# Optimization experiments

Hardware: AMD Instinct MI355X
Metric: run time of the kernel (lower is better)

The kernel has to match this reference:

```python
import jax, jax.numpy as jnp
import numpy as np

B, N, H, KRATE = 128, 400, 128, 0.2
EPS = 1e-9


def setup_inputs() -> dict:
    key = jax.random.key(0)
    ks = jax.random.split(key, 16)
    # correlation-like input: symmetric, values in (-1,1), unit diagonal
    x = jax.random.normal(ks[0], (B, N, N), dtype=jnp.float32)
    x = jnp.tanh(0.3 * x)
    x = 0.5 * (x + x.transpose(0, 2, 1))
    eye = jnp.eye(N, dtype=jnp.float32)
    x = x * (1.0 - eye) + eye

    def lin(k, fan_in, shape):
        return jax.random.normal(k, shape, dtype=jnp.float32) / np.sqrt(fan_in).astype(np.float32)

    return {
        "x": x,
        "slength": jnp.full((B,), 100, dtype=jnp.int32),
        # AE denoiser (num_of_node=N, hidden=H)
        "enc1_w": lin(ks[1], N, (N, H)), "enc1_b": jnp.zeros((H,), jnp.float32),
        "enc2_w": lin(ks[2], N, (N, H)), "enc2_b": jnp.zeros((H,), jnp.float32),
        "dec2_w": lin(ks[3], H, (H, N)), "dec2_b": jnp.zeros((N,), jnp.float32),
        "dec1_w": lin(ks[4], H, (H, N)), "dec1_b": jnp.zeros((N,), jnp.float32),
        # GCN predictor
        "gcn1_w": lin(ks[5], N, (N, H)), "gcn1_b": jnp.zeros((H,), jnp.float32),
        "gcn2_w": lin(ks[6], H, (H, H)), "gcn2_b": jnp.zeros((H,), jnp.float32),
        # classification head Linear(128 -> 2)
        "fc_w": lin(ks[7], H, (H, 2)), "fc_b": jnp.zeros((2,), jnp.float32),
    }


def reference(x, slength, enc1_w, enc1_b, enc2_w, enc2_b, dec2_w, dec2_b,
              dec1_w, dec1_b, gcn1_w, gcn1_b, gcn2_w, gcn2_b, fc_w, fc_b):
    eye = jnp.eye(N, dtype=x.dtype)

    # fisher transform + normalize by [0,0] entry
    xf = 0.5 * jnp.log((1.0 + x + EPS) / (1.0 - x + EPS))
    xf = xf / xf[:, 0, 0][:, None, None]

    # --- DA / AE denoiser: deltax = AE(xf), symmetrized ---
    out1 = jax.nn.relu(jnp.einsum('bij,jh->bih', xf, enc1_w) + enc1_b).transpose(0, 2, 1)  # [B,H,N]
    out2 = jax.nn.relu(jnp.einsum('bhn,nk->bhk', out1, enc2_w) + enc2_b)                   # [B,H,H]
    out2 = jax.nn.relu(jnp.einsum('bhk,kn->bhn', out2, dec2_w) + dec2_b + out1)            # [B,H,N]
    out2 = out2.transpose(0, 2, 1)                                                         # [B,N,H]
    delta = jnp.einsum('bnh,hm->bnm', out2, dec1_w) + dec1_b                               # [B,N,N]
    delta = 0.5 * (delta + delta.transpose(0, 2, 1))
    x2 = xf + delta * (1.0 - eye)

    # --- predictor on detached x2 ---
    xp = jax.lax.stop_gradient(x2)

    # topk sparsification at rate 0.2 over flattened NxN per sample
    k = int(N * N * KRATE)
    flat = xp.reshape(B, N * N)
    _, idx = jax.lax.top_k(flat, k)
    mask = jnp.zeros((B, N * N), xp.dtype).at[jnp.arange(B)[:, None], idx].set(1.0)
    A = xp * mask.reshape(B, N, N)

    # GCN norm (PyG gcn_norm with add_remaining_self_loops, fill=1)
    diag = jnp.diagonal(A, axis1=1, axis2=2)
    A = A + eye[None] * jnp.where(diag == 0.0, 1.0, 0.0)[:, :, None]
    deg = A.sum(axis=1)                      # scatter of edge weight on col index
    dinv = deg ** -0.5
    dinv = jnp.where(jnp.isinf(dinv), 0.0, dinv)
    An = dinv[:, :, None] * A * dinv[:, None, :]  # An[b,i,j] = dinv[i]*A[i,j]*dinv[j]

    # GCNConv1 -> ReLU -> GCNConv2 (aggregate onto col/target index)
    h = jax.nn.relu(jnp.einsum('bij,bif->bjf', An, xp @ gcn1_w) + gcn1_b)  # [B,N,H]
    h = jnp.einsum('bij,bif->bjf', An, h @ gcn2_w) + gcn2_b                # [B,N,H]

    pooled = h.mean(axis=1)                  # mean over nodes -> [B,H]
    out = jax.nn.relu(pooled) @ fc_w + fc_b  # [B,2]
    return out
```

## Files before the change

kernel.cpp:

```cpp
#include <hip/hip_runtime.h>
#include <hip/hip_bf16.h>
#include <math.h>

#define BATCH 128
#define NNODE 400
#define HID   128
#define NN    (NNODE*NNODE)
#define KSEL  32000
#define EQCAP 1024
#define EPSF  1e-9f
#define TSPLIT 8
#define SEG   (NN / TSPLIT)
#define NT    7
#define KC400 14
#define FRAGS (KC400*4096)
#define PLA   57344

__device__ __forceinline__ unsigned tokey(float f) {
  unsigned u = __float_as_uint(f);
  return (u & 0x80000000u) ? ~u : (u | 0x80000000u);
}

__device__ __forceinline__ short f2bf(float f) {
  unsigned u = __float_as_uint(f);
  u += 0x7fffu + ((u >> 16) & 1u);
  return (short)(u >> 16);
}
__device__ __forceinline__ float bf2f(short s) {
  return __uint_as_float(((unsigned)(unsigned short)s) << 16);
}

__device__ __forceinline__ float xfhw(float xv, float cmul) {
  float la = __builtin_amdgcn_logf(1.0f + xv + EPSF);
  float lb = __builtin_amdgcn_logf(1.0f - xv + EPSF);
  return (la - lb) * cmul;
}

typedef __attribute__((ext_vector_type(8))) short s8v;
typedef __attribute__((ext_vector_type(4))) short s4v;
typedef __attribute__((ext_vector_type(4))) float f4v;

#define BK 16
#define LP 68

template<bool AT, bool BIAS, bool RES, bool RELU, bool TS>
__global__ void __launch_bounds__(256) gemm64(
    const float* __restrict__ A, long sA, int lda,
    const float* __restrict__ B, long sB, int ldb,
    const float* __restrict__ bias,
    const float* __restrict__ Res, long sRes,
    float* __restrict__ C, long sC, int ldc,
    int M, int Nc, int K)
{
  __shared__ float As[BK][LP];
  __shared__ float Bs[BK][LP];
  const int bz = blockIdx.z;
  A += (size_t)bz * sA;
  B += (size_t)bz * sB;
  C += (size_t)bz * sC;
  const float* Rp = RES ? (Res + (size_t)bz * sRes) : nullptr;

  const int n0 = blockIdx.x * 64;
  const int m0 = blockIdx.y * 64;
  const int tid = threadIdx.x;
  const int tx = tid & 15, ty = tid >> 4;
  const bool edgeM = (m0 + 64 > M);
  const bool edgeN = (n0 + 64 > Nc);

  float acc[4][4];
#pragma unroll
  for (int i = 0; i < 4; ++i)
#pragma unroll
    for (int j = 0; j < 4; ++j) acc[i][j] = 0.f;

  for (int k0 = 0; k0 < K; k0 += BK) {
    if (!AT) {
      const int m = tid & 63, g = tid >> 6;
      if (!edgeM) {
        const float4 v = *(const float4*)(A + (size_t)(m0 + m) * lda + k0 + 4 * g);
        As[4 * g + 0][m] = v.x; As[4 * g + 1][m] = v.y;
        As[4 * g + 2][m] = v.z; As[4 * g + 3][m] = v.w;
      } else {
        const int gm = m0 + m;
        const bool ok = gm < M;
#pragma unroll
        for (int j = 0; j < 4; ++j)
          As[4 * g + j][m] = ok ? A[(size_t)gm * lda + k0 + 4 * g + j] : 0.f;
      }
    } else {
      const int k = tid >> 4, mg = tid & 15;
      if (!edgeM) {
        const float4 v = *(const float4*)(A + (size_t)(k0 + k) * lda + m0 + 4 * mg);
        *(float4*)&As[k][4 * mg] = v;
      } else {
#pragma unroll
        for (int j = 0; j < 4; ++j) {
          const int gm = m0 + 4 * mg + j;
          As[k][4 * mg + j] = (gm < M) ? A[(size_t)(k0 + k) * lda + gm] : 0.f;
        }
      }
    }
    {
      const int k = tid >> 4, ng = tid & 15;
      if (!edgeN) {
        const float4 v = *(const float4*)(B + (size_t)(k0 + k) * ldb + n0 + 4 * ng);
        *(float4*)&Bs[k][4 * ng] = v;
      } else {
#pragma unroll
        for (int j = 0; j < 4; ++j) {
          const int gn = n0 + 4 * ng + j;
          Bs[k][4 * ng + j] = (gn < Nc) ? B[(size_t)(k0 + k) * ldb + gn] : 0.f;
        }
      }
    }
    __syncthreads();
#pragma unroll
    for (int kk = 0; kk < BK; ++kk) {
      const float4 a = *(const float4*)&As[kk][ty << 2];
      const float4 b = *(const float4*)&Bs[kk][tx << 2];
      const float av[4] = {a.x, a.y, a.z, a.w};
      const float bv[4] = {b.x, b.y, b.z, b.w};
#pragma unroll
      for (int i = 0; i < 4; ++i)
#pragma unroll
        for (int j = 0; j < 4; ++j) acc[i][j] += av[i] * bv[j];
    }
    __syncthreads();
  }

#pragma unroll
  for (int i = 0; i < 4; ++i) {
    const int m = m0 + (ty << 2) + i;
    if (m >= M) continue;
#pragma unroll
    for (int j = 0; j < 4; ++j) {
      const int n = n0 + (tx << 2) + j;
      if (n >= Nc) continue;
      float v = acc[i][j];
      if (BIAS) v += bias[n];
      const size_t loc = TS ? ((size_t)n * ldc + m) : ((size_t)m * ldc + n);
      if (RES) v += Rp[loc];
      if (RELU) v = fmaxf(v, 0.f);
      C[loc] = v;
    }
  }
}

__global__ void bsplit5(
    const float* __restrict__ gcn1_w, const float* __restrict__ gcn2_w,
    const float* __restrict__ enc1_w, const float* __restrict__ enc2_w,
    const float* __restrict__ dec1_w,
    short* __restrict__ w1frag, short* __restrict__ w2frag,
    short* __restrict__ e1frag, short* __restrict__ e2frag,
    short* __restrict__ dfrag) {
  const float* W; short* out; int K, Kpad, N, Npad;
  switch (blockIdx.y) {
    case 0: W = gcn1_w; out = w1frag; K = NNODE; Kpad = 448; N = HID;   Npad = 128; break;
    case 1: W = gcn2_w; out = w2frag; K = HID;   Kpad = 128; N = HID;   Npad = 128; break;
    case 2: W = enc1_w; out = e1frag; K = NNODE; Kpad = 448; N = HID;   Npad = 128; break;
    case 3: W = enc2_w; out = e2frag; K = NNODE; Kpad = 448; N = HID;   Npad = 128; break;
    default: W = dec1_w; out = dfrag; K = HID;   Kpad = 128; N = NNODE; Npad = 448; break;
  }
  int t = blockIdx.x * 256 + threadIdx.x;
  if (t >= Kpad * Npad) return;
  int k = t / Npad, n = t - k * Npad;
  float v = (k < K && n < N) ? W[(size_t)k * N + n] : 0.f;
  short hi = f2bf(v);
  short lo = f2bf(v - bf2f(hi));
  int ntiles = Npad >> 4;
  size_t idx = (((size_t)(k >> 5) * ntiles + (n >> 4)) * 64
                + (((k >> 3) & 3) * 16 + (n & 15))) * 8 + (k & 7);
  size_t PL = (size_t)(Kpad >> 5) * ntiles * 512;
  out[idx] = hi;
  out[PL + idx] = lo;
}

template<bool AT, bool FRAG, bool BIAS, bool RELU, bool SCL, bool TS, bool XF>
__global__ void __launch_bounds__(256) mfgemm(
    const float* __restrict__ A, long sA, int lda,
    const short* __restrict__ Bf, long sB, int kc,
    const float* __restrict__ bias,
    const float* __restrict__ scl,
    float* __restrict__ Cf, long sCf, int ldc,
    short* __restrict__ Cfrag, long sCfrag, int okc,
    const float* __restrict__ denomp, float* __restrict__ xfout,
    int M, int K)
{
  __shared__ float As[64][68];
  const int bz = blockIdx.y;
  A += (size_t)bz * sA;
  Bf += (size_t)bz * sB;
  if (SCL) scl += (size_t)bz * NNODE;
  if (!FRAG) Cf += (size_t)bz * sCf;
  else       Cfrag += (size_t)bz * sCfrag;
  if (XF) xfout += (size_t)bz * sA;
  const float cmul = XF ? (0.34657359027997264f / denomp[bz]) : 0.f;

  const int tid = threadIdx.x;
  const int lane = tid & 63, wave = tid >> 6;
  const int wqm = wave >> 1, wqn = wave & 1;
  const int quad = lane >> 4, l15 = lane & 15;
  const int m0 = blockIdx.x * 64;

  f4v acc[2][4];
#pragma unroll
  for (int i = 0; i < 2; ++i)
#pragma unroll
    for (int j = 0; j < 4; ++j) acc[i][j] = (f4v){0.f, 0.f, 0.f, 0.f};

  const int nstage = (K + 63) >> 6;
  for (int st = 0; st < nstage; ++st) {
    const int k0 = st << 6;
    if (st) __syncthreads();
    if (!AT) {
      const int mrow = tid >> 4;
      const int k4 = (tid & 15) << 2;
#pragma unroll
      for (int u = 0; u < 4; ++u) {
        const int m = mrow + (u << 4);
        const int gm = m0 + m, gk = k0 + k4;
        float4 v = {0.f, 0.f, 0.f, 0.f};
        if (gm < M) {
          if (gk + 4 <= K) {
            float4 xv = *(const float4*)(A + (size_t)gm * lda + gk);
            if (XF) {
              v.x = xfhw(xv.x, cmul);
              v.y = xfhw(xv.y, cmul);
              v.z = xfhw(xv.z, cmul);
              v.w = xfhw(xv.w, cmul);
              *(float4*)(xfout + (size_t)gm * lda + gk) = v;
            } else v = xv;
          } else {
            float* pv = (float*)&v;
#pragma unroll
            for (int j = 0; j < 4; ++j)
              if (gk + j < K) {
                float xv = A[(size_t)gm * lda + gk + j];
                if (XF) {
                  pv[j] = xfhw(xv, cmul);
                  xfout[(size_t)gm * lda + gk + j] = pv[j];
                } else pv[j] = xv;
              }
          }
        }
        *(float4*)&As[m][k4] = v;
      }
    } else {
      const int kk = tid >> 4;
      const int m4 = (tid & 15) << 2;
#pragma unroll
      for (int u = 0; u < 4; ++u) {
        const int gk = k0 + kk + (u << 4);
        float4 v = {0.f, 0.f, 0.f, 0.f};
        if (gk < K) {
          if (m0 + m4 + 4 <= M) v = *(const float4*)(A + (size_t)gk * lda + m0 + m4);
          else {
            float* pv = (float*)&v;
#pragma unroll
            for (int j = 0; j < 4; ++j)
              if (m0 + m4 + j < M) pv[j] = A[(size_t)gk * lda + m0 + m4 + j];
          }
        }
        As[m4 + 0][kk + (u << 4)] = v.x;
        As[m4 + 1][kk + (u << 4)] = v.y;
        As[m4 + 2][kk + (u << 4)] = v.z;
        As[m4 + 3][kk + (u << 4)] = v.w;
      }
    }
    __syncthreads();

#pragma unroll
    for (int c2 = 0; c2 < 2; ++c2) {
      const int c = (st << 1) + c2;
      s8v bhi[4], blo[4];
#pragma unroll
      for (int nt = 0; nt < 4; ++nt) {
        const int ntg = (wqn << 2) + nt;
        const size_t off = (((size_t)c * 8 + ntg) * 64 + lane) * 8;
        bhi[nt] = *(const s8v*)(Bf + off);
        blo[nt] = *(const s8v*)(Bf + (size_t)kc * 4096 + off);
      }
#pragma unroll
      for (int mt = 0; mt < 2; ++mt) {
        const int row = (wqm << 5) + (mt << 4) + l15;
        const int kof = (c2 << 5) + (quad << 3);
        const f4v a0 = *(const f4v*)&As[row][kof];
        const f4v a1 = *(const f4v*)&As[row][kof + 4];
        s8v ah, al;
#pragma unroll
        for (int j = 0; j < 4; ++j) {
          short h0 = f2bf(a0[j]); ah[j] = h0; al[j] = f2bf(a0[j] - bf2f(h0));
          short h1 = f2bf(a1[j]); ah[j + 4] = h1; al[j + 4] = f2bf(a1[j] - bf2f(h1));
        }
#pragma unroll
        for (int nt = 0; nt < 4; ++nt) {
          acc[mt][nt] = __builtin_amdgcn_mfma_f32_16x16x32_bf16(ah, bhi[nt], acc[mt][nt], 0, 0, 0);
          acc[mt][nt] = __builtin_amdgcn_mfma_f32_16x16x32_bf16(ah, blo[nt], acc[mt][nt], 0, 0, 0);
          acc[mt][nt] = __builtin_amdgcn_mfma_f32_16x16x32_bf16(al, bhi[nt], acc[mt][nt], 0, 0, 0);
        }
      }
    }
  }

  if (TS) {
    for (int nh = 0; nh < 2; ++nh) {
      __syncthreads();
      if (wqn == nh) {
#pragma unroll
        for (int mt = 0; mt < 2; ++mt)
#pragma unroll
          for (int nt = 0; nt < 4; ++nt) {
            const int tn = (nt << 4) + l15;
            const int n  = (wqn << 6) + tn;
            const int mc = (wqm << 5) + (mt << 4) + (quad << 2);
            const f4v a = acc[mt][nt];
#pragma unroll
            for (int reg = 0; reg < 4; ++reg) {
              float v = a[reg];
              if (SCL) v *= scl[m0 + mc + reg];
              if (BIAS) v += bias[n];
              if (RELU) v = fmaxf(v, 0.f);
              As[tn][mc + reg] = v;
            }
          }
      }
      __syncthreads();
      const int row = tid >> 2, cq = tid & 3;
#pragma unroll
      for (int u = 0; u < 4; ++u) {
        const int col = (cq + (u << 2)) << 2;
        if (m0 + col + 4 <= M) {
          const float4 v = *(const float4*)&As[row][col];
          *(float4*)(Cf + (size_t)((nh << 6) + row) * ldc + m0 + col) = v;
        }
      }
    }
    return;
  }

#pragma unroll
  for (int mt = 0; mt < 2; ++mt) {
    const int mb = m0 + (wqm << 5) + (mt << 4) + (quad << 2);
#pragma unroll
    for (int nt = 0; nt < 4; ++nt) {
      const int n = (wqn << 6) + (nt << 4) + l15;
      const f4v a = acc[mt][nt];
      if (!FRAG) {
#pragma unroll
        for (int reg = 0; reg < 4; ++reg) {
          const int m = mb + reg;
          if (m < M) {
            float v = a[reg];
            if (SCL) v *= scl[m];
            if (BIAS) v += bias[n];
            if (RELU) v = fmaxf(v, 0.f);
            Cf[(size_t)m * ldc + n] = v;
          }
        }
      } else {
        s4v h4, l4;
#pragma unroll
        for (int reg = 0; reg < 4; ++reg) {
          const int m = mb + reg;
          float v = (m < M) ? (SCL ? a[reg] * scl[m] : a[reg]) : 0.f;
          short hh = f2bf(v);
          h4[reg] = hh; l4[reg] = f2bf(v - bf2f(hh));
        }
        const int chunkT = mb >> 5, quadT = (mb >> 3) & 3, jT0 = mb & 7;
        const size_t off = (((size_t)chunkT * 8 + (wqn << 2) + nt) * 64
                            + quadT * 16 + l15) * 8 + jT0;
        *(s4v*)(Cfrag + off) = h4;
        *(s4v*)(Cfrag + (size_t)okc * 4096 + off) = l4;
      }
    }
  }
}

__global__ void __launch_bounds__(256) g4mf(
    const float* __restrict__ o1,
    const short* __restrict__ wfrag,
    const float* __restrict__ bias,
    float* __restrict__ xf,
    unsigned* __restrict__ ghist)
{
  __shared__ float D2[64][68];
  __shared__ unsigned hist[2048];
  const int b = blockIdx.y;
  int p = blockIdx.x, bi = 0;
  while (p >= NT - bi) { p -= NT - bi; ++bi; }
  const int bj = bi + p;
  const int I0 = bi * 64, J0 = bj * 64;
  const bool diag = (bi == bj);

  o1 += (size_t)b * HID * NNODE;
  xf += (size_t)b * NN;
  unsigned* gh = ghist + (size_t)b * 4096;

  const int tid = threadIdx.x;
  const int lane = tid & 63, wave = tid >> 6;
  const int wq = wave & 1;
  const bool d1 = wave < 2;
  const int Bt = (d1 ? bj : bi) * 4;
  const int quad = lane >> 4, l15 = lane & 15;
  const int M0 = d1 ? I0 : J0;

  for (int i = tid; i < 2048; i += 256) hist[i] = 0u;

  f4v acc[2][4];
#pragma unroll
  for (int i = 0; i < 2; ++i)
#pragma unroll
    for (int j = 0; j < 4; ++j) acc[i][j] = (f4v){0.f, 0.f, 0.f, 0.f};

  const int gm0 = M0 + (wq << 5) + l15;

  for (int c = 0; c < 4; ++c) {
    const int k0 = c << 5;
    s8v bhi[4], blo[4];
#pragma unroll
    for (int nt = 0; nt < 4; ++nt) {
      const int ntg = Bt + nt;
      const size_t off = (((size_t)c * 28 + ntg) * 64 + lane) * 8;
      bhi[nt] = *(const s8v*)(wfrag + off);
      blo[nt] = *(const s8v*)(wfrag + PLA + off);
    }
#pragma unroll
    for (int mt = 0; mt < 2; ++mt) {
      const int gm = gm0 + (mt << 4);
      float av[8];
      if (gm < NNODE) {
        const float* cp = o1 + (size_t)(k0 + (quad << 3)) * NNODE + gm;
#pragma unroll
        for (int j = 0; j < 8; ++j) av[j] = cp[(size_t)j * NNODE];
      } else {
#pragma unroll
        for (int j = 0; j < 8; ++j) av[j] = 0.f;
      }
      s8v ah, al;
#pragma unroll
      for (int j = 0; j < 8; ++j) {
        short h = f2bf(av[j]); ah[j] = h; al[j] = f2bf(av[j] - bf2f(h));
      }
#pragma unroll
      for (int nt = 0; nt < 4; ++nt) {
        acc[mt][nt] = __builtin_amdgcn_mfma_f32_16x16x32_bf16(ah, bhi[nt], acc[mt][nt], 0, 0, 0);
        acc[mt][nt] = __builtin_amdgcn_mfma_f32_16x16x32_bf16(ah, blo[nt], acc[mt][nt], 0, 0, 0);
        acc[mt][nt] = __builtin_amdgcn_mfma_f32_16x16x32_bf16(al, bhi[nt], acc[mt][nt], 0, 0, 0);
      }
    }
  }

  if (!d1) {
#pragma unroll
    for (int mt = 0; mt < 2; ++mt) {
      const int mb = (wq << 5) + (mt << 4) + (quad << 2);
#pragma unroll
      for (int nt = 0; nt < 4; ++nt) {
        const int nn = (nt << 4) + l15;
        const f4v a = acc[mt][nt];
#pragma unroll
        for (int reg = 0; reg < 4; ++reg) D2[mb + reg][nn] = a[reg];
      }
    }
  }
  __syncthreads();

  if (d1) {
    const unsigned w = diag ? 1u : 2u;
#pragma unroll
    for (int mt = 0; mt < 2; ++mt) {
      const int a0 = (wq << 5) + (mt << 4) + (quad << 2);
#pragma unroll
      for (int nt = 0; nt < 4; ++nt) {
        const int nn = (nt << 4) + l15;
        const int gj = J0 + nn;
        const f4v d1v = acc[mt][nt];
        const f4v d2t = *(const f4v*)&D2[nn][a0];
        f4v vv;
#pragma unroll
        for (int reg = 0; reg < 4; ++reg) {
          const int gi = I0 + a0 + reg;
          float v = 0.f;
          if (gi < NNODE && gj < NNODE) {
            v = xf[(size_t)gi * NNODE + gj];
            if (gi != gj)
              v += 0.5f * (d1v[reg] + d2t[reg] + bias[gj] + bias[gi]);
            const unsigned bin = tokey(v) >> 20;
            atomicAdd(&hist[bin >> 1], w << ((bin & 1) << 4));
          }
          vv[reg] = v;
        }
#pragma unroll
        for (int reg = 0; reg < 4; ++reg) {
          const int gi = I0 + a0 + reg;
          if (gi < NNODE && gj < NNODE) xf[(size_t)gi * NNODE + gj] = vv[reg];
        }
        if (!diag && gj < NNODE && (I0 + a0 + 4 <= NNODE)) {
          *(float4*)(xf + (size_t)gj * NNODE + I0 + a0) = *(float4*)&vv;
        }
      }
    }
  }
  __syncthreads();
  for (int i = tid; i < 2048; i += 256) {
    const unsigned v = hist[i];
    const unsigned lo = v & 0xFFFFu, hi = v >> 16;
    if (lo) atomicAdd(&gh[2 * i], lo);
    if (hi) atomicAdd(&gh[2 * i + 1], hi);
  }
}

__global__ void tzd(const float* __restrict__ x, unsigned* __restrict__ ghist,
                    unsigned* __restrict__ sprefix, int* __restrict__ sk,
                    int* __restrict__ eqcnt, float* __restrict__ deg,
                    float* __restrict__ denom, unsigned* __restrict__ ccnt2) {
  int t = blockIdx.x * 256 + threadIdx.x;
  if (t < BATCH * 4096) ghist[t] = 0u;
  if (t < BATCH) {
    sprefix[t] = 0u; sk[t] = KSEL; eqcnt[t] = 0;
    float v = x[(size_t)t * NN];
    denom[t] = 0.5f * logf((1.0f + v + EPSF) / (1.0f - v + EPSF));
  }
  if (t < BATCH * TSPLIT) ccnt2[t] = 0u;
  if (t < BATCH * NNODE) deg[t] = 0.f;
}

__global__ void __launch_bounds__(256) thistA(const float* __restrict__ x2,
                                              const unsigned* __restrict__ sprefix,
                                              unsigned* __restrict__ ghist,
                                              unsigned* __restrict__ cand,
                                              unsigned* __restrict__ ccnt2) {
  __shared__ unsigned h[4096];
  __shared__ unsigned lcnt;
  const int b  = blockIdx.y;
  const int sb = blockIdx.x;
  const int tid = threadIdx.x;
  for (int i = tid; i < 4096; i += 256) h[i] = 0u;
  if (tid == 0) lcnt = 0u;
  __syncthreads();

  const unsigned prefix = sprefix[b];
  unsigned* cb = cand + (size_t)b * NN + (size_t)sb * SEG;
  const float4* p4 = (const float4*)(x2 + (size_t)b * NN);
  const int i0 = sb * (SEG / 4), i1 = i0 + (SEG / 4);
  for (int i = i0 + tid; i < i1; i += 256) {
    float4 v = p4[i];
    unsigned kk[4] = {tokey(v.x), tokey(v.y), tokey(v.z), tokey(v.w)};
#pragma unroll
    for (int q = 0; q < 4; ++q) {
      const unsigned key = kk[q];
      if ((key & 0xFFF00000u) == prefix) {
        atomicAdd(&h[(key >> 8) & 4095u], 1u);
        const unsigned pos = atomicAdd(&lcnt, 1u);
        cb[pos] = key;
      }
    }
  }
  __syncthreads();
  for (int i = tid; i < 4096; i += 256) {
    unsigned s = h[i];
    if (s) atomicAdd(&ghist[(size_t)b * 4096 + i], s);
  }
  if (tid == 0) ccnt2[b * TSPLIT + sb] = lcnt;
}

template<int SH>
__global__ void __launch_bounds__(256) tpick12(unsigned* __restrict__ ghist,
                                               unsigned* __restrict__ sprefix,
                                               int* __restrict__ sk) {
  const int b = blockIdx.x;
  __shared__ unsigned h[4096];
  __shared__ unsigned csum[256];
  unsigned* gh = ghist + (size_t)b * 4096;
  unsigned local = 0;
#pragma unroll
  for (int u = 0; u < 16; ++u) {
    unsigned v = gh[threadIdx.x * 16 + u];
    h[threadIdx.x * 16 + u] = v;
    local += v;
  }
  csum[threadIdx.x] = local;
  __syncthreads();
  if (threadIdx.x == 0) {
    int k = sk[b];
    int bin = 0;
    for (int ch = 255; ch >= 0; --ch) {
      int S = (int)csum[ch];
      if (S >= k) {
        for (int bb = ch * 16 + 15; bb >= ch * 16; --bb) {
          int c = (int)h[bb];
          if (c >= k) { bin = bb; break; }
          k -= c;
        }
        break;
      }
      k -= S;
    }
    sprefix[b] = sprefix[b] | ((unsigned)bin << SH);
    sk[b] = k;
  }
#pragma unroll
  for (int u = 0; u < 16; ++u) gh[threadIdx.x * 16 + u] = 0u;
}

__global__ void __launch_bounds__(256) thistC(const unsigned* __restrict__ cand,
                                              const unsigned* __restrict__ ccnt2,
                                              const unsigned* __restrict__ sprefix,
                                              const int* __restrict__ sk,
                                              unsigned* __restrict__ tau,
                                              int* __restrict__ rrem) {
  __shared__ unsigned h[8][256];
  const int b = blockIdx.x;
  const int tid = threadIdx.x;
  for (int i = tid; i < 8 * 256; i += 256) ((unsigned*)h)[i] = 0u;
  __syncthreads();
  const unsigned prefix = sprefix[b];
  const int rep = tid & 7;
  for (int sb = 0; sb < TSPLIT; ++sb) {
    const unsigned n = ccnt2[b * TSPLIT + sb];
    const unsigned* cp = cand + (size_t)b * NN + (size_t)sb * SEG;
    for (unsigned i = tid; i < n; i += 256) {
      const unsigned key = cp[i];
      if ((key & 0xFFFFFF00u) == prefix) atomicAdd(&h[rep][key & 255u], 1u);
    }
  }
  __syncthreads();
  if (tid < 256) {
    const unsigned s = h[0][tid] + h[1][tid] + h[2][tid] + h[3][tid]
                     + h[4][tid] + h[5][tid] + h[6][tid] + h[7][tid];
    h[0][tid] = s;
  }
  __syncthreads();
  if (tid == 0) {
    int k = sk[b];
    unsigned byte = 0u;
    for (int bin = 255; bin >= 0; --bin) {
      int c = (int)h[0][bin];
      if (c >= k) { byte = (unsigned)bin; break; }
      k -= c;
    }
    tau[b] = prefix | byte;
    rrem[b] = k;
  }
}

__global__ void __launch_bounds__(256) build_kc(
    const float* __restrict__ x2, const unsigned* __restrict__ tau,
    float* __restrict__ A, float* __restrict__ deg,
    int* __restrict__ eqcnt, int* __restrict__ eqidx) {
  __shared__ float cs[NNODE];
  const int b = blockIdx.y, rg = blockIdx.x;
  const int tid = threadIdx.x;
  for (int i = tid; i < NNODE; i += 256) cs[i] = 0.f;
  __syncthreads();
  const unsigned tk = tau[b];
  const size_t base = (size_t)b * NN + (size_t)rg * 6400;
  for (int u = 0; u < 25; ++u) {
    const int t = u * 256 + tid;
    const float v = x2[base + t];
    const unsigned key = tokey(v);
    const float a = (key > tk) ? v : 0.f;
    A[base + t] = a;
    if (key == tk) {
      int p = atomicAdd(&eqcnt[b], 1);
      if (p < EQCAP) eqidx[b * EQCAP + p] = rg * 6400 + t;
    }
    if (a != 0.f) atomicAdd(&cs[t % NNODE], a);
  }
  __syncthreads();
  for (int j = tid; j < NNODE; j += 256)
    if (cs[j] != 0.f) atomicAdd(&deg[b * NNODE + j], cs[j]);
}

__global__ void __launch_bounds__(256) eqdinv(
    float* __restrict__ A, const float* __restrict__ x2,
    float* __restrict__ deg, float* __restrict__ dinv,
    const int* __restrict__ eqcnt, const int* __restrict__ eqidx,
    const int* __restrict__ rrem) {
  const int b = blockIdx.x;
  int cnt = eqcnt[b]; if (cnt > EQCAP) cnt = EQCAP;
  const int r = rrem[b];
  for (int t = threadIdx.x; t < cnt; t += 256) {
    int idx = eqidx[b * EQCAP + t];
    int rank = 0;
    for (int u = 0; u < cnt; ++u) rank += (eqidx[b * EQCAP + u] < idx) ? 1 : 0;
    if (rank < r) {
      float v = x2[(size_t)b * NN + idx];
      A[(size_t)b * NN + idx] = v;
      atomicAdd(&deg[b * NNODE + idx % NNODE], v);
    }
  }
  __syncthreads();
  for (int j = threadIdx.x; j < NNODE; j += 256) {
    float d = deg[b * NNODE + j];
    size_t o = (size_t)b * NN + (size_t)j * NNODE + j;
    if (A[o] == 0.f) { A[o] = 1.0f; d += 1.0f; }
    dinv[b * NNODE + j] = (d == 0.f) ? 0.f : 1.0f / sqrtf(d);
  }
}

__global__ void head_k(const float* __restrict__ h2, const float* __restrict__ fc_w,
                       const float* __restrict__ fc_b, float* __restrict__ out) {
  int b = blockIdx.x;
  int f = threadIdx.x;
  float s = 0.f;
  const float* p = h2 + (size_t)b * NNODE * HID + f;
  for (int j = 0; j < NNODE; ++j) s += p[(size_t)j * HID];
  float pv = fmaxf(s / (float)NNODE, 0.f);
  __shared__ float r0[128], r1[128];
  r0[f] = pv * fc_w[f * 2 + 0];
  r1[f] = pv * fc_w[f * 2 + 1];
  __syncthreads();
  for (int sft = 64; sft > 0; sft >>= 1) {
    if (f < sft) { r0[f] += r0[f + sft]; r1[f] += r1[f + sft]; }
    __syncthreads();
  }
  if (f == 0) {
    out[b * 2 + 0] = r0[0] + fc_b[0];
    out[b * 2 + 1] = r1[0] + fc_b[1];
  }
}

extern "C" void kernel_launch(void* const* d_in, const int* in_sizes, int n_in,
                              void* d_out, int out_size, void* d_ws, size_t ws_size,
                              hipStream_t stream) {
  const float* x      = (const float*)d_in[0];
  const float* enc1_w = (const float*)d_in[2];
  const float* enc1_b = (const float*)d_in[3];
  const float* enc2_w = (const float*)d_in[4];
  const float* enc2_b = (const float*)d_in[5];
  const float* dec2_w = (const float*)d_in[6];
  const float* dec2_b = (const float*)d_in[7];
  const float* dec1_w = (const float*)d_in[8];
  const float* dec1_b = (const float*)d_in[9];
  const float* gcn1_w = (const float*)d_in[10];
  const float* gcn1_b = (const float*)d_in[11];
  const float* gcn2_w = (const float*)d_in[12];
  const float* gcn2_b = (const float*)d_in[13];
  const float* fc_w   = (const float*)d_in[14];
  const float* fc_b   = (const float*)d_in[15];
  float* out = (float*)d_out;
  (void)in_sizes; (void)n_in; (void)out_size; (void)ws_size;

  float* ws = (float*)d_ws;
  size_t off = 0;
  auto take = [&](size_t n) { float* p = ws + off; off += (n + 63) & ~(size_t)63; return p; };
  float* xf   = take((size_t)BATCH * NN);
  float* dl   = take((size_t)BATCH * NN);
  float* o1   = take((size_t)BATCH * HID * NNODE);
  float* o2   = take((size_t)BATCH * HID * HID);
  float* hbuf = take((size_t)BATCH * NNODE * HID);
  float* denom = take(BATCH);
  float* dinv  = take((size_t)BATCH * NNODE);
  float* deg   = take((size_t)BATCH * NNODE);
  unsigned* tau = (unsigned*)take(BATCH);
  int* rrem  = (int*)take(BATCH);
  int* eqcnt = (int*)take(BATCH);
  int* eqidx = (int*)take((size_t)BATCH * EQCAP);
  unsigned* ghist   = (unsigned*)take((size_t)BATCH * 4096);
  unsigned* sprefix = (unsigned*)take(BATCH);
  int*      sk      = (int*)take(BATCH);
  unsigned* ccnt2   = (unsigned*)take((size_t)BATCH * TSPLIT);
  short* w1frag = (short*)take((size_t)FRAGS + 64);
  short* w2frag = (short*)take((size_t)4 * 4096 + 64);
  short* e1frag = (short*)take((size_t)FRAGS + 64);
  short* e2frag = (short*)take((size_t)FRAGS + 64);
  short* dfrag  = (short*)take((size_t)PLA + 64);
  short* xwfrag = (short*)o1;
  unsigned* cand = (unsigned*)dl;
  const long sXW = 2L * FRAGS;

  tzd<<<2048, 256, 0, stream>>>(x, ghist, sprefix, sk, eqcnt, deg, denom, ccnt2);
  bsplit5<<<dim3(224, 5), 256, 0, stream>>>(gcn1_w, gcn2_w, enc1_w, enc2_w, dec1_w,
                                            w1frag, w2frag, e1frag, e2frag, dfrag);

  mfgemm<false, false, true, true, false, true, true><<<dim3(7, BATCH), 256, 0, stream>>>(
      x, NN, NNODE, e1frag, 0, KC400, enc1_b, nullptr,
      o1, (long)HID * NNODE, NNODE, nullptr, 0, 0, denom, xf, NNODE, NNODE);
  mfgemm<false, false, true, true, false, false, false><<<dim3(2, BATCH), 256, 0, stream>>>(
      o1, (long)HID * NNODE, NNODE, e2frag, 0, KC400, enc2_b, nullptr,
      o2, (long)HID * HID, HID, nullptr, 0, 0, nullptr, nullptr, HID, NNODE);
  gemm64<false, true, true, true, false><<<dim3(7, 2, BATCH), 256, 0, stream>>>(
      o2, (long)HID * HID, HID, dec2_w, 0, NNODE, dec2_b,
      o1, (long)HID * NNODE, o1, (long)HID * NNODE, NNODE, HID, NNODE, HID);

  g4mf<<<dim3(NT * (NT + 1) / 2, BATCH), 256, 0, stream>>>(o1, dfrag, dec1_b, xf, ghist);

  tpick12<20><<<BATCH, 256, 0, stream>>>(ghist, sprefix, sk);
  thistA<<<dim3(TSPLIT, BATCH), 256, 0, stream>>>(xf, sprefix, ghist, cand, ccnt2);
  tpick12<8><<<BATCH, 256, 0, stream>>>(ghist, sprefix, sk);
  thistC<<<BATCH, 256, 0, stream>>>(cand, ccnt2, sprefix, sk, tau, rrem);

  build_kc<<<dim3(25, BATCH), 256, 0, stream>>>(xf, tau, dl, deg, eqcnt, eqidx);
  eqdinv<<<BATCH, 256, 0, stream>>>(dl, xf, deg, dinv, eqcnt, eqidx, rrem);

  mfgemm<false, true, false, false, true, false, false><<<dim3(7, BATCH), 256, 0, stream>>>(
      xf, NN, NNODE, w1frag, 0, KC400, nullptr, dinv,
      nullptr, 0, 128, xwfrag, sXW, KC400, nullptr, nullptr, NNODE, NNODE);
  mfgemm<true, false, true, true, true, false, false><<<dim3(7, BATCH), 256, 0, stream>>>(
      dl, NN, NNODE, xwfrag, sXW, KC400, gcn1_b, dinv,
      hbuf, (long)NNODE * HID, HID, nullptr, 0, 0, nullptr, nullptr, NNODE, NNODE);
  mfgemm<false, true, false, false, true, false, false><<<dim3(7, BATCH), 256, 0, stream>>>(
      hbuf, (long)NNODE * HID, HID, w2frag, 0, 4, nullptr, dinv,
      nullptr, 0, 128, xwfrag, sXW, KC400, nullptr, nullptr, NNODE, HID);
  mfgemm<true, false, true, false, true, false, false><<<dim3(7, BATCH), 256, 0, stream>>>(
      dl, NN, NNODE, xwfrag, sXW, KC400, gcn2_b, dinv,
      hbuf, (long)NNODE * HID, HID, nullptr, 0, 0, nullptr, nullptr, NNODE, NNODE);

  head_k<<<BATCH, HID, 0, stream>>>(hbuf, fc_w, fc_b, out);
}
```

Before: 694.2 us.

## Fuse top-k mask build and degree accumulation into the X·W1 GEMM load

Removes the separate build_kc pass by doing the threshold masking, tie collection and per-column degree accumulation inside the A-tile load of the xf·W1 GEMM, since that GEMM already streams all of xf. The dinv row scaling that this GEMM used to apply is moved to the A-operand load of the aggregation GEMMs (DSCL), because dinv is not yet available when the fused kernel runs. This saves one full read of the x2 matrix and a launch. In exchange the GEMM does atomics during tile loads and the later GEMMs do extra multiplies.

```diff
diff --git a/kernel.cpp b/kernel.cpp
--- a/kernel.cpp
+++ b/kernel.cpp
@@ -175,7 +175,8 @@
   out[PL + idx] = lo;
 }
 
-template<bool AT, bool FRAG, bool BIAS, bool RELU, bool SCL, bool TS, bool XF>
+template<bool AT, bool FRAG, bool BIAS, bool RELU, bool SCL, bool TS, bool XF,
+         bool MASK, bool DSCL>
 __global__ void __launch_bounds__(256) mfgemm(
     const float* __restrict__ A, long sA, int lda,
     const short* __restrict__ Bf, long sB, int kc,
@@ -184,9 +185,13 @@
     float* __restrict__ Cf, long sCf, int ldc,
     short* __restrict__ Cfrag, long sCfrag, int okc,
     const float* __restrict__ denomp, float* __restrict__ xfout,
+    const unsigned* __restrict__ taup, float* __restrict__ Aout,
+    float* __restrict__ degp, int* __restrict__ eqcntp,
+    int* __restrict__ eqidxp, const float* __restrict__ dsclp,
     int M, int K)
 {
   __shared__ float As[64][68];
+  __shared__ float cs[MASK ? NNODE : 1];
   const int bz = blockIdx.y;
   A += (size_t)bz * sA;
   Bf += (size_t)bz * sB;
@@ -195,12 +200,21 @@
   else       Cfrag += (size_t)bz * sCfrag;
   if (XF) xfout += (size_t)bz * sA;
   const float cmul = XF ? (0.34657359027997264f / denomp[bz]) : 0.f;
+  const unsigned tk = MASK ? taup[bz] : 0u;
+  if (MASK) { Aout += (size_t)bz * NN; degp += (size_t)bz * NNODE;
+              eqcntp += bz; eqidxp += (size_t)bz * EQCAP; }
+  if (DSCL) dsclp += (size_t)bz * NNODE;
 
   const int tid = threadIdx.x;
   const int lane = tid & 63, wave = tid >> 6;
   const int wqm = wave >> 1, wqn = wave & 1;
   const int quad = lane >> 4, l15 = lane & 15;
   const int m0 = blockIdx.x * 64;
+
+  if (MASK) {
+    for (int i = tid; i < NNODE; i += 256) cs[i] = 0.f;
+    __syncthreads();
+  }
 
   f4v acc[2][4];
 #pragma unroll
@@ -230,6 +244,23 @@
               v.w = xfhw(xv.w, cmul);
               *(float4*)(xfout + (size_t)gm * lda + gk) = v;
             } else v = xv;
+            if (MASK) {
+              float4 av;
+              float* pa = (float*)&av;
+              const float* px = (const float*)&v;
+#pragma unroll
+              for (int j = 0; j < 4; ++j) {
+                const unsigned key = tokey(px[j]);
+                float a = (key > tk) ? px[j] : 0.f;
+                if (key == tk) {
+                  int p = atomicAdd(eqcntp, 1);
+                  if (p < EQCAP) eqidxp[p] = gm * NNODE + gk + j;
+                }
+                if (a != 0.f) atomicAdd(&cs[gk + j], a);
+                pa[j] = a;
+              }
+              *(float4*)(Aout + (size_t)gm * NNODE + gk) = av;
+            }
           } else {
             float* pv = (float*)&v;
 #pragma unroll
@@ -240,6 +271,16 @@
                   pv[j] = xfhw(xv, cmul);
                   xfout[(size_t)gm * lda + gk + j] = pv[j];
                 } else pv[j] = xv;
+                if (MASK) {
+                  const unsigned key = tokey(pv[j]);
+                  float a = (key > tk) ? pv[j] : 0.f;
+                  if (key == tk) {
+                    int p = atomicAdd(eqcntp, 1);
+                    if (p < EQCAP) eqidxp[p] = gm * NNODE + gk + j;
+                  }
+                  if (a != 0.f) atomicAdd(&cs[gk + j], a);
+                  Aout[(size_t)gm * NNODE + gk + j] = a;
+                }
               }
           }
         }
@@ -253,12 +294,18 @@
         const int gk = k0 + kk + (u << 4);
         float4 v = {0.f, 0.f, 0.f, 0.f};
         if (gk < K) {
-          if (m0 + m4 + 4 <= M) v = *(const float4*)(A + (size_t)gk * lda + m0 + m4);
-          else {
+          const float ds = DSCL ? dsclp[gk] : 1.f;
+          if (m0 + m4 + 4 <= M) {
+            v = *(const float4*)(A + (size_t)gk * lda + m0 + m4);
+            if (DSCL) { v.x *= ds; v.y *= ds; v.z *= ds; v.w *= ds; }
+          } else {
             float* pv = (float*)&v;
 #pragma unroll
             for (int j = 0; j < 4; ++j)
-              if (m0 + m4 + j < M) pv[j] = A[(size_t)gk * lda + m0 + m4 + j];
+              if (m0 + m4 + j < M) {
+                float t = A[(size_t)gk * lda + m0 + m4 + j];
+                pv[j] = DSCL ? t * ds : t;
+              }
           }
         }
         As[m4 + 0][kk + (u << 4)] = v.x;
@@ -299,6 +346,14 @@
           acc[mt][nt] = __builtin_amdgcn_mfma_f32_16x16x32_bf16(al, bhi[nt], acc[mt][nt], 0, 0, 0);
         }
       }
+    }
+  }
+
+  if (MASK) {
+    __syncthreads();
+    for (int j = tid; j < NNODE; j += 256) {
+      const float s = cs[j];
+      if (s != 0.f) atomicAdd(&degp[j], s);
     }
   }
 
@@ -642,34 +697,6 @@
     tau[b] = prefix | byte;
     rrem[b] = k;
   }
-}
-
-__global__ void __launch_bounds__(256) build_kc(
-    const float* __restrict__ x2, const unsigned* __restrict__ tau,
-    float* __restrict__ A, float* __restrict__ deg,
-    int* __restrict__ eqcnt, int* __restrict__ eqidx) {
-  __shared__ float cs[NNODE];
-  const int b = blockIdx.y, rg = blockIdx.x;
-  const int tid = threadIdx.x;
-  for (int i = tid; i < NNODE; i += 256) cs[i] = 0.f;
-  __syncthreads();
-  const unsigned tk = tau[b];
-  const size_t base = (size_t)b * NN + (size_t)rg * 6400;
-  for (int u = 0; u < 25; ++u) {
-    const int t = u * 256 + tid;
-    const float v = x2[base + t];
-    const unsigned key = tokey(v);
-    const float a = (key > tk) ? v : 0.f;
-    A[base + t] = a;
-    if (key == tk) {
-      int p = atomicAdd(&eqcnt[b], 1);
-      if (p < EQCAP) eqidx[b * EQCAP + p] = rg * 6400 + t;
-    }
-    if (a != 0.f) atomicAdd(&cs[t % NNODE], a);
-  }
-  __syncthreads();
-  for (int j = tid; j < NNODE; j += 256)
-    if (cs[j] != 0.f) atomicAdd(&deg[b * NNODE + j], cs[j]);
 }
 
 __global__ void __launch_bounds__(256) eqdinv(
@@ -774,12 +801,14 @@
   bsplit5<<<dim3(224, 5), 256, 0, stream>>>(gcn1_w, gcn2_w, enc1_w, enc2_w, dec1_w,
                                             w1frag, w2frag, e1frag, e2frag, dfrag);
 
-  mfgemm<false, false, true, true, false, true, true><<<dim3(7, BATCH), 256, 0, stream>>>(
+  mfgemm<false, false, true, true, false, true, true, false, false><<<dim3(7, BATCH), 256, 0, stream>>>(
       x, NN, NNODE, e1frag, 0, KC400, enc1_b, nullptr,
-      o1, (long)HID * NNODE, NNODE, nullptr, 0, 0, denom, xf, NNODE, NNODE);
-  mfgemm<false, false, true, true, false, false, false><<<dim3(2, BATCH), 256, 0, stream>>>(
+      o1, (long)HID * NNODE, NNODE, nullptr, 0, 0, denom, xf,
+      nullptr, nullptr, nullptr, nullptr, nullptr, nullptr, NNODE, NNODE);
+  mfgemm<false, false, true, true, false, false, false, false, false><<<dim3(2, BATCH), 256, 0, stream>>>(
       o1, (long)HID * NNODE, NNODE, e2frag, 0, KC400, enc2_b, nullptr,
-      o2, (long)HID * HID, HID, nullptr, 0, 0, nullptr, nullptr, HID, NNODE);
+      o2, (long)HID * HID, HID, nullptr, 0, 0, nullptr, nullptr,
+      nullptr, nullptr, nullptr, nullptr, nullptr, nullptr, HID, NNODE);
   gemm64<false, true, true, true, false><<<dim3(7, 2, BATCH), 256, 0, stream>>>(
       o2, (long)HID * HID, HID, dec2_w, 0, NNODE, dec2_b,
       o1, (long)HID * NNODE, o1, (long)HID * NNODE, NNODE, HID, NNODE, HID);
@@ -791,21 +820,24 @@
   tpick12<8><<<BATCH, 256, 0, stream>>>(ghist, sprefix, sk);
   thistC<<<BATCH, 256, 0, stream>>>(cand, ccnt2, sprefix, sk, tau, rrem);
 
-  build_kc<<<dim3(25, BATCH), 256, 0, stream>>>(xf, tau, dl, deg, eqcnt, eqidx);
+  mfgemm<false, true, false, false, false, false, false, true, false><<<dim3(7, BATCH), 256, 0, stream>>>(
+      xf, NN, NNODE, w1frag, 0, KC400, nullptr, nullptr,
+      nullptr, 0, 128, xwfrag, sXW, KC400, nullptr, nullptr,
+      tau, dl, deg, eqcnt, eqidx, nullptr, NNODE, NNODE);
   eqdinv<<<BATCH, 256, 0, stream>>>(dl, xf, deg, dinv, eqcnt, eqidx, rrem);
 
-  mfgemm<false, true, false, false, true, false, false><<<dim3(7, BATCH), 256, 0, stream>>>(
-      xf, NN, NNODE, w1frag, 0, KC400, nullptr, dinv,
-      nullptr, 0, 128, xwfrag, sXW, KC400, nullptr, nullptr, NNODE, NNODE);
-  mfgemm<true, false, true, true, true, false, false><<<dim3(7, BATCH), 256, 0, stream>>>(
+  mfgemm<true, false, true, true, true, false, false, false, true><<<dim3(7, BATCH), 256, 0, stream>>>(
       dl, NN, NNODE, xwfrag, sXW, KC400, gcn1_b, dinv,
-      hbuf, (long)NNODE * HID, HID, nullptr, 0, 0, nullptr, nullptr, NNODE, NNODE);
-  mfgemm<false, true, false, false, true, false, false><<<dim3(7, BATCH), 256, 0, stream>>>(
-      hbuf, (long)NNODE * HID, HID, w2frag, 0, 4, nullptr, dinv,
-      nullptr, 0, 128, xwfrag, sXW, KC400, nullptr, nullptr, NNODE, HID);
-  mfgemm<true, false, true, false, true, false, false><<<dim3(7, BATCH), 256, 0, stream>>>(
+      hbuf, (long)NNODE * HID, HID, nullptr, 0, 0, nullptr, nullptr,
+      nullptr, nullptr, nullptr, nullptr, nullptr, dinv, NNODE, NNODE);
+  mfgemm<false, true, false, false, false, false, false, false, false><<<dim3(7, BATCH), 256, 0, stream>>>(
+      hbuf, (long)NNODE * HID, HID, w2frag, 0, 4, nullptr, nullptr,
+      nullptr, 0, 128, xwfrag, sXW, KC400, nullptr, nullptr,
+      nullptr, nullptr, nullptr, nullptr, nullptr, nullptr, NNODE, HID);
+  mfgemm<true, false, true, false, true, false, false, false, true><<<dim3(7, BATCH), 256, 0, stream>>>(
       dl, NN, NNODE, xwfrag, sXW, KC400, gcn2_b, dinv,
-      hbuf, (long)NNODE * HID, HID, nullptr, 0, 0, nullptr, nullptr, NNODE, NNODE);
+      hbuf, (long)NNODE * HID, HID, nullptr, 0, 0, nullptr, nullptr,
+      nullptr, nullptr, nullptr, nullptr, nullptr, dinv, NNODE, NNODE);
 
   head_k<<<BATCH, HID, 0, stream>>>(hbuf, fc_w, fc_b, out);
 }
```

Result: faster. 634.9 us (-8.5%).
